# Kernel optimization log

Hardware: AMD Instinct MI355X
Metric: run time of the kernel (lower is better)

The kernel has to match this reference:

```python
import jax, jax.numpy as jnp
import numpy as np

D = 1024      # in_dim
HS = 64       # head_size
H = 16        # num_heads
B, S = 2, 2048


def setup_inputs() -> dict:
    key = jax.random.key(0)
    k1, k2, k3, k4, k5, k6 = jax.random.split(key, 6)
    scale = 1.0 / np.sqrt(D)
    x = jax.random.normal(k1, (B, S, D), dtype=jnp.float32)
    # Stacked per-head projection weights (torch Linear weight is [out,in];
    # random init so layout only needs to be consistent). query weight exists
    # in the torch module but is never used (source bug), so it is omitted.
    Wk = jax.random.normal(k2, (H, D, HS), dtype=jnp.float32) * scale
    Wv = jax.random.normal(k3, (H, D, HS), dtype=jnp.float32) * scale
    Wproj = jax.random.normal(k4, (H * HS, D), dtype=jnp.float32) * (1.0 / np.sqrt(H * HS))
    bproj = jax.random.normal(k5, (D,), dtype=jnp.float32) * 0.01
    return {"x": x, "Wk": Wk, "Wv": Wv, "Wproj": Wproj, "bproj": bproj}


def reference(x, Wk, Wv, Wproj, bproj):
    # Faithful to source: k = key(x); q = value(x); v = value(x)  (q == v, no softmax)
    k = jnp.einsum("bsd,hde->bhse", x, Wk)   # [B,H,S,HS]
    v = jnp.einsum("bsd,hde->bhse", x, Wv)   # [B,H,S,HS]
    q = v
    inv_sqrt = jnp.asarray(HS, x.dtype) ** -0.5
    wei = jnp.einsum("bhse,bhte->bhst", q, k) * inv_sqrt  # [B,H,S,S], unnormalized
    out = jnp.einsum("bhst,bhte->bhse", wei, v)            # [B,H,S,HS]
    # concat heads: [B,S,H*HS]
    out = jnp.transpose(out, (0, 2, 1, 3)).reshape(x.shape[0], x.shape[1], H * HS)
    return out @ Wproj + bproj  # [B,S,D]
```

## Files before the change

### kernel.cpp

```cpp
#include <hip/hip_runtime.h>

#define B_ 2
#define S_ 2048
#define D_ 1024
#define H_ 16
#define HS_ 64
#define HD_ 1024
#define BS_ (B_*S_)
#define KS_ 64
#define TP2_ 264

typedef __attribute__((ext_vector_type(8))) short short8_t;
typedef __attribute__((ext_vector_type(4))) float float4_t;

__device__ inline unsigned short f32_to_bf16(float f) {
  unsigned int u = __float_as_uint(f);
  u += 0x7FFF + ((u >> 16) & 1);
  return (unsigned short)(u >> 16);
}

__device__ inline void async_copy16(const void* g, void* lds) {
  __builtin_amdgcn_global_load_lds(
      (const __attribute__((address_space(1))) void*)g,
      (__attribute__((address_space(3))) void*)lds, 16, 0, 0);
}

#define WAITV6 asm volatile("s_waitcnt vmcnt(6)" ::: "memory")
#define WAITV4 asm volatile("s_waitcnt vmcnt(4)" ::: "memory")
#define WAITV0 asm volatile("s_waitcnt vmcnt(0)" ::: "memory")
#define WAITL0 asm volatile("s_waitcnt lgkmcnt(0)" ::: "memory")
#define BAR    __builtin_amdgcn_s_barrier()
#define SCHEDB __builtin_amdgcn_sched_barrier(0)
#define PRIO1  __builtin_amdgcn_s_setprio(1)
#define PRIO0  __builtin_amdgcn_s_setprio(0)


__global__ __launch_bounds__(256) void prep_kernel(
    const float* __restrict__ x, const float* __restrict__ Wk,
    const float* __restrict__ Wv, unsigned short* __restrict__ xb,
    unsigned short* __restrict__ Wkvt) {
  const int blk = blockIdx.x;
  const int tid = threadIdx.x;
  __shared__ float lds[64][65];
  if (blk < 4096) {
    int idx = blk * 256 + tid;
    float4 v = ((const float4*)x)[idx];
    ushort4 o;
    o.x = f32_to_bf16(v.x); o.y = f32_to_bf16(v.y);
    o.z = f32_to_bf16(v.z); o.w = f32_to_bf16(v.w);
    ((ushort4*)xb)[idx] = o;
    return;
  }
  const int wblk = blk - 4096;
  const int h = wblk >> 4;
  const int d0 = (wblk & 15) * 64;
#pragma unroll
  for (int i = 0; i < 16; ++i) {
    int idx = tid + i * 256; int dd = idx >> 6, e = idx & 63;
    lds[e][dd] = Wk[((size_t)h * D_ + d0 + dd) * HS_ + e];
  }
  __syncthreads();
#pragma unroll
  for (int i = 0; i < 16; ++i) {
    int idx = tid + i * 256; int e = idx >> 6, dd = idx & 63;
    Wkvt[((size_t)h * 128 + e) * D_ + d0 + dd] = f32_to_bf16(lds[e][dd]);
  }
  __syncthreads();
#pragma unroll
  for (int i = 0; i < 16; ++i) {
    int idx = tid + i * 256; int dd = idx >> 6, e = idx & 63;
    lds[e][dd] = Wv[((size_t)h * D_ + d0 + dd) * HS_ + e];
  }
  __syncthreads();
#pragma unroll
  for (int i = 0; i < 16; ++i) {
    int idx = tid + i * 256; int e = idx >> 6, dd = idx & 63;
    Wkvt[((size_t)h * 128 + 64 + e) * D_ + d0 + dd] = f32_to_bf16(lds[e][dd]);
  }
}

__global__ __launch_bounds__(512) void kv_mfma_kernel(
    const unsigned short* __restrict__ xb,
    const unsigned short* __restrict__ Wkvt,
    unsigned short* __restrict__ Vb,
    float* __restrict__ Mpart) {
  const int blk = blockIdx.x;
  const int stile = blk & 15;
  const int h = blk >> 4;
  const int s0 = stile * 256;
  const int tid = threadIdx.x;
  const int lane = tid & 63;
  const int wid = tid >> 6;
  const int wm = wid >> 1, wn = wid & 1;
  const int quad = lane >> 4, l16 = lane & 15;
  const int xa = l16 & 7;

  __shared__ __align__(16) unsigned char smem[147456];
  unsigned short* const Ktl = (unsigned short*)smem;
  unsigned short* const Vtl = (unsigned short*)(smem + 64 * TP2_ * 2);

  float4_t acc[4][4];
  const float4_t fz = {0.f, 0.f, 0.f, 0.f};
#pragma unroll
  for (int i = 0; i < 4; ++i)
#pragma unroll
    for (int j = 0; j < 4; ++j) acc[i][j] = fz;

  unsigned short* pc = (unsigned short*)(smem);
  unsigned short* pn = (unsigned short*)(smem + 49152);
  unsigned short* ps = (unsigned short*)(smem + 98304);

  auto stageu = [&](unsigned short* slot, int kt, int u) {
    const int k0 = kt * KS_;
    if (u < 4) {
      int rb = u * 64 + wid * 8;
      int r = rb + (lane >> 3);
      int ch = ((lane & 7) ^ (r & 7)) * 8;
      async_copy16(xb + (size_t)(s0 + r) * D_ + k0 + ch, slot + rb * KS_);
    } else {
      int rb = (u - 4) * 64 + wid * 8;
      int r = rb + (lane >> 3);
      int ch = ((lane & 7) ^ (r & 7)) * 8;
      async_copy16(Wkvt + ((size_t)h * 128 + r) * D_ + k0 + ch,
                   slot + 16384 + rb * KS_);
    }
  };
  auto rdA = [&](const unsigned short* P, int mi, int ks) {
    return *(const short8_t*)(P + (wm * 64 + mi * 16 + l16) * KS_ +
                              ((ks * 4 + quad) ^ xa) * 8);
  };
  auto rdB = [&](const unsigned short* P, int ni, int ks) {
    return *(const short8_t*)(P + 16384 + (wn * 64 + ni * 16 + l16) * KS_ +
                              ((ks * 4 + quad) ^ xa) * 8);
  };

  short8_t a0[4], a1[4], b0[4], b1[4];

#pragma unroll
  for (int u = 0; u < 6; ++u) stageu(pc, 0, u);
#pragma unroll
  for (int u = 0; u < 6; ++u) stageu(pn, 1, u);
  WAITV6;
  BAR;
#pragma unroll
  for (int mi = 0; mi < 4; ++mi) a0[mi] = rdA(pc, mi, 0);
  b0[0] = rdB(pc, 0, 0); b0[1] = rdB(pc, 1, 0);

  for (int kt = 0; kt < 16; ++kt) {
    const bool st = (kt < 14);
    if (st) { stageu(ps, kt + 2, 0); stageu(ps, kt + 2, 1); }
    BAR; WAITL0; SCHEDB;
    PRIO1;
#pragma unroll
    for (int mi = 0; mi < 4; ++mi) {
      acc[mi][0] = __builtin_amdgcn_mfma_f32_16x16x32_bf16(a0[mi], b0[0], acc[mi][0], 0, 0, 0);
      acc[mi][1] = __builtin_amdgcn_mfma_f32_16x16x32_bf16(a0[mi], b0[1], acc[mi][1], 0, 0, 0);
    }
    PRIO0;
    b0[2] = rdB(pc, 2, 0); b0[3] = rdB(pc, 3, 0);
    if (st) { stageu(ps, kt + 2, 2); stageu(ps, kt + 2, 3); }
    BAR; WAITL0; SCHEDB;
    PRIO1;
#pragma unroll
    for (int mi = 0; mi < 4; ++mi) {
      acc[mi][2] = __builtin_amdgcn_mfma_f32_16x16x32_bf16(a0[mi], b0[2], acc[mi][2], 0, 0, 0);
      acc[mi][3] = __builtin_amdgcn_mfma_f32_16x16x32_bf16(a0[mi], b0[3], acc[mi][3], 0, 0, 0);
    }
    PRIO0;
#pragma unroll
    for (int mi = 0; mi < 4; ++mi) a1[mi] = rdA(pc, mi, 1);
    b1[0] = rdB(pc, 0, 1); b1[1] = rdB(pc, 1, 1);
    if (st) stageu(ps, kt + 2, 4);
    BAR; WAITL0; SCHEDB;
    PRIO1;
#pragma unroll
    for (int mi = 0; mi < 4; ++mi) {
      acc[mi][0] = __builtin_amdgcn_mfma_f32_16x16x32_bf16(a1[mi], b1[0], acc[mi][0], 0, 0, 0);
      acc[mi][1] = __builtin_amdgcn_mfma_f32_16x16x32_bf16(a1[mi], b1[1], acc[mi][1], 0, 0, 0);
    }
    PRIO0;
    b1[2] = rdB(pc, 2, 1); b1[3] = rdB(pc, 3, 1);
    if (st) stageu(ps, kt + 2, 5);
    if (kt < 14) { WAITV6; } else if (kt == 14) { WAITV0; }
    BAR; WAITL0; SCHEDB;
    PRIO1;
#pragma unroll
    for (int mi = 0; mi < 4; ++mi) {
      acc[mi][2] = __builtin_amdgcn_mfma_f32_16x16x32_bf16(a1[mi], b1[2], acc[mi][2], 0, 0, 0);
      acc[mi][3] = __builtin_amdgcn_mfma_f32_16x16x32_bf16(a1[mi], b1[3], acc[mi][3], 0, 0, 0);
    }
    PRIO0;
    if (kt < 15) {
#pragma unroll
      for (int mi = 0; mi < 4; ++mi) a0[mi] = rdA(pn, mi, 0);
      b0[0] = rdB(pn, 0, 0); b0[1] = rdB(pn, 1, 0);
    }
    unsigned short* t = pc; pc = pn; pn = ps; ps = t;
  }
  __syncthreads();

  {
    unsigned short* dstT = (wn == 0) ? Ktl : Vtl;
#pragma unroll
    for (int mi = 0; mi < 4; ++mi)
#pragma unroll
      for (int ni = 0; ni < 4; ++ni) {
        int f = ni * 16 + l16;
        int sm = wm * 64 + mi * 16 + quad * 4;
        ushort4 o;
        o.x = f32_to_bf16(acc[mi][ni][0]);
        o.y = f32_to_bf16(acc[mi][ni][1]);
        o.z = f32_to_bf16(acc[mi][ni][2]);
        o.w = f32_to_bf16(acc[mi][ni][3]);
        *(ushort4*)&dstT[f * TP2_ + sm] = o;
      }
  }
  __syncthreads();

#pragma unroll
  for (int u = 0; u < 4; ++u) {
    int unit = tid + u * 512;
    int s = unit & 255;
    int ec = (unit >> 8) * 8;
    union { unsigned short u16[8]; uint4 v; } tv;
#pragma unroll
    for (int e = 0; e < 8; ++e) tv.u16[e] = Vtl[(ec + e) * TP2_ + s];
    *(uint4*)&Vb[(size_t)(s0 + s) * HD_ + h * 64 + ec] = tv.v;
  }

  {
    const int half = wid >> 2, fq = wid & 3;
    float4_t macc[4];
#pragma unroll
    for (int ni = 0; ni < 4; ++ni) macc[ni] = fz;
#pragma unroll
    for (int ss = 0; ss < 4; ++ss) {
      short8_t ka = *(const short8_t*)&Ktl[(fq * 16 + l16) * TP2_ +
                                           half * 128 + ss * 32 + quad * 8];
#pragma unroll
      for (int ni = 0; ni < 4; ++ni) {
        short8_t vv = *(const short8_t*)&Vtl[(ni * 16 + l16) * TP2_ +
                                             half * 128 + ss * 32 + quad * 8];
        macc[ni] = __builtin_amdgcn_mfma_f32_16x16x32_bf16(ka, vv, macc[ni], 0, 0, 0);
      }
    }
    float* mdst = Mpart + (((size_t)(stile * 2 + half)) * H_ + h) * 4096;
#pragma unroll
    for (int ni = 0; ni < 4; ++ni) {
      int e = ni * 16 + l16;
#pragma unroll
      for (int r = 0; r < 4; ++r) {
        int f = fq * 16 + quad * 4 + r;
        mdst[f * 64 + e] = macc[ni][r];
      }
    }
  }
}

__global__ __launch_bounds__(256) void m_reduce_kernel(
    const float* __restrict__ Mpart, float* __restrict__ M) {
  const int gid = blockIdx.x * 256 + threadIdx.x;
  const int e0 = gid * 4;
  const int bh = e0 >> 12;
  const int idx = e0 & 4095;
  const int b = bh >> 4, h = bh & 15;
  float4 s = {0.f, 0.f, 0.f, 0.f};
#pragma unroll
  for (int p = 0; p < 16; ++p) {
    const float4 v =
        *(const float4*)&Mpart[(((size_t)(b * 16 + p)) * H_ + h) * 4096 + idx];
    s.x += v.x; s.y += v.y; s.z += v.z; s.w += v.w;
  }
  s.x *= 0.125f; s.y *= 0.125f; s.z *= 0.125f; s.w *= 0.125f;
  *(float4*)&M[(size_t)bh * 4096 + idx] = s;
}

__global__ __launch_bounds__(256) void p_kernel(
    const float* __restrict__ M, const float* __restrict__ Wproj,
    unsigned short* __restrict__ Pt) {
  const int blk = blockIdx.x;
  const int dtile = blk & 15;
  const int h = (blk >> 4) & 15;
  const int b = blk >> 8;
  const int d0 = dtile * 64;
  const int tid = threadIdx.x;
  const int tx = tid & 15, ty = tid >> 4;
  __shared__ float Ms[64][68];
  __shared__ float Ws[64][68];
  const size_t mbase = ((size_t)(b * H_ + h)) * HS_ * HS_;
#pragma unroll
  for (int i = 0; i < 16; ++i) {
    int idx = tid + i * 256;
    int f = idx >> 6, e = idx & 63;
    Ms[e][f] = M[mbase + idx];
    Ws[f][e] = Wproj[(size_t)(h * HS_ + f) * D_ + d0 + e];
  }
  __syncthreads();
  float acc[4][4] = {};
#pragma unroll
  for (int kk = 0; kk < 64; ++kk) {
    const float4 a4 = *(const float4*)&Ms[kk][ty * 4];
    const float4 b4 = *(const float4*)&Ws[kk][tx * 4];
    const float a[4] = {a4.x, a4.y, a4.z, a4.w};
    const float bb[4] = {b4.x, b4.y, b4.z, b4.w};
#pragma unroll
    for (int i = 0; i < 4; ++i)
#pragma unroll
      for (int j = 0; j < 4; ++j) acc[i][j] += a[i] * bb[j];
  }
  __syncthreads();
#pragma unroll
  for (int i = 0; i < 4; ++i)
#pragma unroll
    for (int j = 0; j < 4; ++j)
      Ms[tx * 4 + j][ty * 4 + i] = acc[i][j];
  __syncthreads();
  {
    int c = tid >> 2, ch = tid & 3;
    unsigned short* dst = Pt + ((size_t)(b * D_ + d0 + c)) * HD_ + h * 64 + ch * 16;
#pragma unroll
    for (int e = 0; e < 16; ++e) dst[e] = f32_to_bf16(Ms[c][ch * 16 + e]);
  }
}

__global__ __launch_bounds__(512) void out_mfma_kernel(
    const unsigned short* __restrict__ Vb,
    const unsigned short* __restrict__ Pt,
    const float* __restrict__ bproj,
    float* __restrict__ out) {
  const int blk = blockIdx.x;
  const int ntile = blk & 7;
  const int stile = blk >> 3;
  const int s0 = stile * 128;
  const int n0 = ntile * 128;
  const int b = s0 >> 11;
  const int tid = threadIdx.x;
  const int lane = tid & 63;
  const int wid = tid >> 6;
  const int wm = wid & 1, wn = wid >> 1;
  const int quad = lane >> 4, l16 = lane & 15;
  const int xa = l16 & 7;

  __shared__ __align__(16) unsigned char smem[98304];

  float4_t acc[4][2];
  const float4_t fz = {0.f, 0.f, 0.f, 0.f};
#pragma unroll
  for (int i = 0; i < 4; ++i)
#pragma unroll
    for (int j = 0; j < 2; ++j) acc[i][j] = fz;

  const unsigned short* Bpanel = Pt + (size_t)b * D_ * HD_;

  unsigned short* pc = (unsigned short*)(smem);
  unsigned short* pn = (unsigned short*)(smem + 32768);
  unsigned short* ps = (unsigned short*)(smem + 65536);

  auto stageu = [&](unsigned short* slot, int kt, int u) {
    const int k0 = kt * KS_;
    if (u < 2) {
      int rb = u * 64 + wid * 8;
      int r = rb + (lane >> 3);
      int ch = ((lane & 7) ^ (r & 7)) * 8;
      async_copy16(Vb + (size_t)(s0 + r) * HD_ + k0 + ch, slot + rb * KS_);
    } else {
      int rb = (u - 2) * 64 + wid * 8;
      int r = rb + (lane >> 3);
      int ch = ((lane & 7) ^ (r & 7)) * 8;
      async_copy16(Bpanel + (size_t)(n0 + r) * HD_ + k0 + ch,
                   slot + 8192 + rb * KS_);
    }
  };
  auto rdA = [&](const unsigned short* P, int mi, int ks) {
    return *(const short8_t*)(P + (wm * 64 + mi * 16 + l16) * KS_ +
                              ((ks * 4 + quad) ^ xa) * 8);
  };
  auto rdB = [&](const unsigned short* P, int ni, int ks) {
    return *(const short8_t*)(P + 8192 + (wn * 32 + ni * 16 + l16) * KS_ +
                              ((ks * 4 + quad) ^ xa) * 8);
  };

  short8_t a0[4], a1[4], b0[2], b1[2];

#pragma unroll
  for (int u = 0; u < 4; ++u) stageu(pc, 0, u);
#pragma unroll
  for (int u = 0; u < 4; ++u) stageu(pn, 1, u);
  WAITV4;
  BAR;
#pragma unroll
  for (int mi = 0; mi < 4; ++mi) a0[mi] = rdA(pc, mi, 0);
  b0[0] = rdB(pc, 0, 0); b0[1] = rdB(pc, 1, 0);

  for (int kt = 0; kt < 16; ++kt) {
    const bool st = (kt < 14);
    if (st) { stageu(ps, kt + 2, 0); stageu(ps, kt + 2, 1); }
    BAR; WAITL0; SCHEDB;
    PRIO1;
#pragma unroll
    for (int mi = 0; mi < 4; ++mi) {
      acc[mi][0] = __builtin_amdgcn_mfma_f32_16x16x32_bf16(a0[mi], b0[0], acc[mi][0], 0, 0, 0);
      acc[mi][1] = __builtin_amdgcn_mfma_f32_16x16x32_bf16(a0[mi], b0[1], acc[mi][1], 0, 0, 0);
    }
    PRIO0;
#pragma unroll
    for (int mi = 0; mi < 4; ++mi) a1[mi] = rdA(pc, mi, 1);
    b1[0] = rdB(pc, 0, 1); b1[1] = rdB(pc, 1, 1);
    if (st) { stageu(ps, kt + 2, 2); stageu(ps, kt + 2, 3); }
    if (kt < 14) { WAITV4; } else if (kt == 14) { WAITV0; }
    BAR; WAITL0; SCHEDB;
    PRIO1;
#pragma unroll
    for (int mi = 0; mi < 4; ++mi) {
      acc[mi][0] = __builtin_amdgcn_mfma_f32_16x16x32_bf16(a1[mi], b1[0], acc[mi][0], 0, 0, 0);
      acc[mi][1] = __builtin_amdgcn_mfma_f32_16x16x32_bf16(a1[mi], b1[1], acc[mi][1], 0, 0, 0);
    }
    PRIO0;
    if (kt < 15) {
#pragma unroll
      for (int mi = 0; mi < 4; ++mi) a0[mi] = rdA(pn, mi, 0);
      b0[0] = rdB(pn, 0, 0); b0[1] = rdB(pn, 1, 0);
    }
    unsigned short* t = pc; pc = pn; pn = ps; ps = t;
  }

#pragma unroll
  for (int ni = 0; ni < 2; ++ni) {
    int col = n0 + wn * 32 + ni * 16 + l16;
    float bias = bproj[col];
#pragma unroll
    for (int mi = 0; mi < 4; ++mi) {
      int rowb = s0 + wm * 64 + mi * 16 + quad * 4;
#pragma unroll
      for (int r = 0; r < 4; ++r)
        out[(size_t)(rowb + r) * D_ + col] = acc[mi][ni][r] + bias;
    }
  }
}

extern "C" void kernel_launch(void* const* d_in, const int* in_sizes, int n_in,
                              void* d_out, int out_size, void* d_ws, size_t ws_size,
                              hipStream_t stream) {
  const float* x = (const float*)d_in[0];
  const float* Wk = (const float*)d_in[1];
  const float* Wv = (const float*)d_in[2];
  const float* Wproj = (const float*)d_in[3];
  const float* bproj = (const float*)d_in[4];
  float* out = (float*)d_out;

  char* ws = (char*)d_ws;
  unsigned short* xb = (unsigned short*)ws;
  unsigned short* Wkvt = xb + (size_t)BS_ * D_;
  unsigned short* Vb = Wkvt + (size_t)H_ * 128 * D_;
  float* Mpart = (float*)(Vb + (size_t)BS_ * HD_);
  float* M = Mpart + (size_t)32 * H_ * 4096;
  unsigned short* Pt = (unsigned short*)(M + (size_t)B_ * H_ * 4096);

  prep_kernel<<<dim3(4096 + H_ * (D_ / 64)), dim3(256), 0, stream>>>(x, Wk, Wv, xb, Wkvt);
  kv_mfma_kernel<<<dim3(16 * H_), dim3(512), 0, stream>>>(xb, Wkvt, Vb, Mpart);
  m_reduce_kernel<<<dim3(128), dim3(256), 0, stream>>>(Mpart, M);
  p_kernel<<<dim3(B_ * H_ * (D_ / 64)), dim3(256), 0, stream>>>(M, Wproj, Pt);
  out_mfma_kernel<<<dim3(32 * 8), dim3(512), 0, stream>>>(Vb, Pt, bproj, out);
}
```

Baseline: 129.0 us.

## Fuse five kernels into one cooperative persistent kernel with grid syncs

Merges the prep, KV projection, M reduction, P computation and output GEMM kernels into one cooperative launch of 256 blocks of 512 threads, with grid.sync() between stages. Each stage's work is remapped onto the fixed grid, for example the prep stage now loops over 8 chunks per thread and the P stage runs two virtual blocks per workgroup. This removes four kernel launch boundaries and their drain and fill gaps. In exchange it adds grid-wide barrier cost and lower parallelism in the lightweight stages, and it needs all 256 blocks to be co-resident, each holding 147 KB of LDS.

```diff
diff --git a/kernel.cpp b/kernel.cpp
--- a/kernel.cpp
+++ b/kernel.cpp
@@ -1,4 +1,7 @@
 #include <hip/hip_runtime.h>
+#include <hip/hip_cooperative_groups.h>
+
+namespace cg = cooperative_groups;
 
 #define B_ 2
 #define S_ 2048
@@ -35,405 +38,405 @@
 #define PRIO0  __builtin_amdgcn_s_setprio(0)
 
 
-__global__ __launch_bounds__(256) void prep_kernel(
+__global__ __launch_bounds__(512) void fused_kernel(
     const float* __restrict__ x, const float* __restrict__ Wk,
-    const float* __restrict__ Wv, unsigned short* __restrict__ xb,
-    unsigned short* __restrict__ Wkvt) {
+    const float* __restrict__ Wv, const float* __restrict__ Wproj,
+    const float* __restrict__ bproj,
+    unsigned short* __restrict__ xb,
+    unsigned short* __restrict__ Wkvt,
+    unsigned short* __restrict__ Vb,
+    float* __restrict__ Mpart,
+    float* __restrict__ M,
+    unsigned short* __restrict__ Pt,
+    float* __restrict__ out) {
   const int blk = blockIdx.x;
   const int tid = threadIdx.x;
-  __shared__ float lds[64][65];
-  if (blk < 4096) {
-    int idx = blk * 256 + tid;
-    float4 v = ((const float4*)x)[idx];
-    ushort4 o;
-    o.x = f32_to_bf16(v.x); o.y = f32_to_bf16(v.y);
-    o.z = f32_to_bf16(v.z); o.w = f32_to_bf16(v.w);
-    ((ushort4*)xb)[idx] = o;
-    return;
+  __shared__ __align__(16) unsigned char smem[147456];
+  cg::grid_group grid = cg::this_grid();
+
+  {
+#pragma unroll
+    for (int u = 0; u < 8; ++u) {
+      int idx = (blk * 512 + tid) + u * 131072;
+      float4 v = ((const float4*)x)[idx];
+      ushort4 o;
+      o.x = f32_to_bf16(v.x); o.y = f32_to_bf16(v.y);
+      o.z = f32_to_bf16(v.z); o.w = f32_to_bf16(v.w);
+      ((ushort4*)xb)[idx] = o;
+    }
+    float (*lds)[65] = (float(*)[65])smem;
+    const int h = blk >> 4;
+    const int d0 = (blk & 15) * 64;
+#pragma unroll
+    for (int i = 0; i < 8; ++i) {
+      int idx = tid + i * 512; int dd = idx >> 6, e = idx & 63;
+      lds[e][dd] = Wk[((size_t)h * D_ + d0 + dd) * HS_ + e];
+    }
+    __syncthreads();
+#pragma unroll
+    for (int i = 0; i < 8; ++i) {
+      int idx = tid + i * 512; int e = idx >> 6, dd = idx & 63;
+      Wkvt[((size_t)h * 128 + e) * D_ + d0 + dd] = f32_to_bf16(lds[e][dd]);
+    }
+    __syncthreads();
+#pragma unroll
+    for (int i = 0; i < 8; ++i) {
+      int idx = tid + i * 512; int dd = idx >> 6, e = idx & 63;
+      lds[e][dd] = Wv[((size_t)h * D_ + d0 + dd) * HS_ + e];
+    }
+    __syncthreads();
+#pragma unroll
+    for (int i = 0; i < 8; ++i) {
+      int idx = tid + i * 512; int e = idx >> 6, dd = idx & 63;
+      Wkvt[((size_t)h * 128 + 64 + e) * D_ + d0 + dd] = f32_to_bf16(lds[e][dd]);
+    }
   }
-  const int wblk = blk - 4096;
-  const int h = wblk >> 4;
-  const int d0 = (wblk & 15) * 64;
-#pragma unroll
-  for (int i = 0; i < 16; ++i) {
-    int idx = tid + i * 256; int dd = idx >> 6, e = idx & 63;
-    lds[e][dd] = Wk[((size_t)h * D_ + d0 + dd) * HS_ + e];
+  grid.sync();
+
+  {
+    const int stile = blk & 15;
+    const int h = blk >> 4;
+    const int s0 = stile * 256;
+    const int lane = tid & 63;
+    const int wid = tid >> 6;
+    const int wm = wid >> 1, wn = wid & 1;
+    const int quad = lane >> 4, l16 = lane & 15;
+    const int xa = l16 & 7;
+
+    unsigned short* const Ktl = (unsigned short*)smem;
+    unsigned short* const Vtl = (unsigned short*)(smem + 64 * TP2_ * 2);
+
+    float4_t acc[4][4];
+    const float4_t fz = {0.f, 0.f, 0.f, 0.f};
+#pragma unroll
+    for (int i = 0; i < 4; ++i)
+#pragma unroll
+      for (int j = 0; j < 4; ++j) acc[i][j] = fz;
+
+    unsigned short* pc = (unsigned short*)(smem);
+    unsigned short* pn = (unsigned short*)(smem + 49152);
+    unsigned short* ps = (unsigned short*)(smem + 98304);
+
+    auto stageu = [&](unsigned short* slot, int kt, int u) {
+      const int k0 = kt * KS_;
+      if (u < 4) {
+        int rb = u * 64 + wid * 8;
+        int r = rb + (lane >> 3);
+        int ch = ((lane & 7) ^ (r & 7)) * 8;
+        async_copy16(xb + (size_t)(s0 + r) * D_ + k0 + ch, slot + rb * KS_);
+      } else {
+        int rb = (u - 4) * 64 + wid * 8;
+        int r = rb + (lane >> 3);
+        int ch = ((lane & 7) ^ (r & 7)) * 8;
+        async_copy16(Wkvt + ((size_t)h * 128 + r) * D_ + k0 + ch,
+                     slot + 16384 + rb * KS_);
+      }
+    };
+    auto rdA = [&](const unsigned short* P, int mi, int ks) {
+      return *(const short8_t*)(P + (wm * 64 + mi * 16 + l16) * KS_ +
+                                ((ks * 4 + quad) ^ xa) * 8);
+    };
+    auto rdB = [&](const unsigned short* P, int ni, int ks) {
+      return *(const short8_t*)(P + 16384 + (wn * 64 + ni * 16 + l16) * KS_ +
+                                ((ks * 4 + quad) ^ xa) * 8);
+    };
+
+    short8_t a0[4], a1[4], b0[4], b1[4];
+
+#pragma unroll
+    for (int u = 0; u < 6; ++u) stageu(pc, 0, u);
+#pragma unroll
+    for (int u = 0; u < 6; ++u) stageu(pn, 1, u);
+    WAITV6;
+    BAR;
+#pragma unroll
+    for (int mi = 0; mi < 4; ++mi) a0[mi] = rdA(pc, mi, 0);
+    b0[0] = rdB(pc, 0, 0); b0[1] = rdB(pc, 1, 0);
+
+    for (int kt = 0; kt < 16; ++kt) {
+      const bool st = (kt < 14);
+      if (st) { stageu(ps, kt + 2, 0); stageu(ps, kt + 2, 1); }
+      BAR; WAITL0; SCHEDB;
+      PRIO1;
+#pragma unroll
+      for (int mi = 0; mi < 4; ++mi) {
+        acc[mi][0] = __builtin_amdgcn_mfma_f32_16x16x32_bf16(a0[mi], b0[0], acc[mi][0], 0, 0, 0);
+        acc[mi][1] = __builtin_amdgcn_mfma_f32_16x16x32_bf16(a0[mi], b0[1], acc[mi][1], 0, 0, 0);
+      }
+      PRIO0;
+      b0[2] = rdB(pc, 2, 0); b0[3] = rdB(pc, 3, 0);
+      if (st) { stageu(ps, kt + 2, 2); stageu(ps, kt + 2, 3); }
+      BAR; WAITL0; SCHEDB;
+      PRIO1;
+#pragma unroll
+      for (int mi = 0; mi < 4; ++mi) {
+        acc[mi][2] = __builtin_amdgcn_mfma_f32_16x16x32_bf16(a0[mi], b0[2], acc[mi][2], 0, 0, 0);
+        acc[mi][3] = __builtin_amdgcn_mfma_f32_16x16x32_bf16(a0[mi], b0[3], acc[mi][3], 0, 0, 0);
+      }
+      PRIO0;
+#pragma unroll
+      for (int mi = 0; mi < 4; ++mi) a1[mi] = rdA(pc, mi, 1);
+      b1[0] = rdB(pc, 0, 1); b1[1] = rdB(pc, 1, 1);
+      if (st) stageu(ps, kt + 2, 4);
+      BAR; WAITL0; SCHEDB;
+      PRIO1;
+#pragma unroll
+      for (int mi = 0; mi < 4; ++mi) {
+        acc[mi][0] = __builtin_amdgcn_mfma_f32_16x16x32_bf16(a1[mi], b1[0], acc[mi][0], 0, 0, 0);
+        acc[mi][1] = __builtin_amdgcn_mfma_f32_16x16x32_bf16(a1[mi], b1[1], acc[mi][1], 0, 0, 0);
+      }
+      PRIO0;
+      b1[2] = rdB(pc, 2, 1); b1[3] = rdB(pc, 3, 1);
+      if (st) stageu(ps, kt + 2, 5);
+      if (kt < 14) { WAITV6; } else if (kt == 14) { WAITV0; }
+      BAR; WAITL0; SCHEDB;
+      PRIO1;
+#pragma unroll
+      for (int mi = 0; mi < 4; ++mi) {
+        acc[mi][2] = __builtin_amdgcn_mfma_f32_16x16x32_bf16(a1[mi], b1[2], acc[mi][2], 0, 0, 0);
+        acc[mi][3] = __builtin_amdgcn_mfma_f32_16x16x32_bf16(a1[mi], b1[3], acc[mi][3], 0, 0, 0);
+      }
+      PRIO0;
+      if (kt < 15) {
+#pragma unroll
+        for (int mi = 0; mi < 4; ++mi) a0[mi] = rdA(pn, mi, 0);
+        b0[0] = rdB(pn, 0, 0); b0[1] = rdB(pn, 1, 0);
+      }
+      unsigned short* t = pc; pc = pn; pn = ps; ps = t;
+    }
+    __syncthreads();
+
+    {
+      unsigned short* dstT = (wn == 0) ? Ktl : Vtl;
+#pragma unroll
+      for (int mi = 0; mi < 4; ++mi)
+#pragma unroll
+        for (int ni = 0; ni < 4; ++ni) {
+          int f = ni * 16 + l16;
+          int sm = wm * 64 + mi * 16 + quad * 4;
+          ushort4 o;
+          o.x = f32_to_bf16(acc[mi][ni][0]);
+          o.y = f32_to_bf16(acc[mi][ni][1]);
+          o.z = f32_to_bf16(acc[mi][ni][2]);
+          o.w = f32_to_bf16(acc[mi][ni][3]);
+          *(ushort4*)&dstT[f * TP2_ + sm] = o;
+        }
+    }
+    __syncthreads();
+
+#pragma unroll
+    for (int u = 0; u < 4; ++u) {
+      int unit = tid + u * 512;
+      int s = unit & 255;
+      int ec = (unit >> 8) * 8;
+      union { unsigned short u16[8]; uint4 v; } tv;
+#pragma unroll
+      for (int e = 0; e < 8; ++e) tv.u16[e] = Vtl[(ec + e) * TP2_ + s];
+      *(uint4*)&Vb[(size_t)(s0 + s) * HD_ + h * 64 + ec] = tv.v;
+    }
+
+    {
+      const int half = wid >> 2, fq = wid & 3;
+      float4_t macc[4];
+#pragma unroll
+      for (int ni = 0; ni < 4; ++ni) macc[ni] = fz;
+#pragma unroll
+      for (int ss = 0; ss < 4; ++ss) {
+        short8_t ka = *(const short8_t*)&Ktl[(fq * 16 + l16) * TP2_ +
+                                             half * 128 + ss * 32 + quad * 8];
+#pragma unroll
+        for (int ni = 0; ni < 4; ++ni) {
+          short8_t vv = *(const short8_t*)&Vtl[(ni * 16 + l16) * TP2_ +
+                                               half * 128 + ss * 32 + quad * 8];
+          macc[ni] = __builtin_amdgcn_mfma_f32_16x16x32_bf16(ka, vv, macc[ni], 0, 0, 0);
+        }
+      }
+      float* mdst = Mpart + (((size_t)(stile * 2 + half)) * H_ + h) * 4096;
+#pragma unroll
+      for (int ni = 0; ni < 4; ++ni) {
+        int e = ni * 16 + l16;
+#pragma unroll
+        for (int r = 0; r < 4; ++r) {
+          int f = fq * 16 + quad * 4 + r;
+          mdst[f * 64 + e] = macc[ni][r];
+        }
+      }
+    }
   }
-  __syncthreads();
-#pragma unroll
-  for (int i = 0; i < 16; ++i) {
-    int idx = tid + i * 256; int e = idx >> 6, dd = idx & 63;
-    Wkvt[((size_t)h * 128 + e) * D_ + d0 + dd] = f32_to_bf16(lds[e][dd]);
+  grid.sync();
+
+  {
+    int gid = blk * 512 + tid;
+    if (gid < 32768) {
+      const int e0 = gid * 4;
+      const int bh = e0 >> 12;
+      const int idx = e0 & 4095;
+      const int b = bh >> 4, h = bh & 15;
+      float4 s = {0.f, 0.f, 0.f, 0.f};
+#pragma unroll
+      for (int p = 0; p < 16; ++p) {
+        const float4 v =
+            *(const float4*)&Mpart[(((size_t)(b * 16 + p)) * H_ + h) * 4096 + idx];
+        s.x += v.x; s.y += v.y; s.z += v.z; s.w += v.w;
+      }
+      s.x *= 0.125f; s.y *= 0.125f; s.z *= 0.125f; s.w *= 0.125f;
+      *(float4*)&M[(size_t)bh * 4096 + idx] = s;
+    }
   }
-  __syncthreads();
-#pragma unroll
-  for (int i = 0; i < 16; ++i) {
-    int idx = tid + i * 256; int dd = idx >> 6, e = idx & 63;
-    lds[e][dd] = Wv[((size_t)h * D_ + d0 + dd) * HS_ + e];
+  grid.sync();
+
+  {
+    const int sel = tid >> 8;
+    const int tid2 = tid & 255;
+    const int vb = blk * 2 + sel;
+    const int dtile = vb & 15;
+    const int h = (vb >> 4) & 15;
+    const int b = vb >> 8;
+    const int d0 = dtile * 64;
+    const int tx = tid2 & 15, ty = tid2 >> 4;
+    float (*Ms)[68] = (float(*)[68])(smem + (size_t)sel * 34816);
+    float (*Ws)[68] = (float(*)[68])(smem + (size_t)sel * 34816 + 17408);
+    const size_t mbase = ((size_t)(b * H_ + h)) * HS_ * HS_;
+#pragma unroll
+    for (int i = 0; i < 16; ++i) {
+      int idx = tid2 + i * 256;
+      int f = idx >> 6, e = idx & 63;
+      Ms[e][f] = M[mbase + idx];
+      Ws[f][e] = Wproj[(size_t)(h * HS_ + f) * D_ + d0 + e];
+    }
+    __syncthreads();
+    float acc[4][4] = {};
+#pragma unroll
+    for (int kk = 0; kk < 64; ++kk) {
+      const float4 a4 = *(const float4*)&Ms[kk][ty * 4];
+      const float4 b4 = *(const float4*)&Ws[kk][tx * 4];
+      const float a[4] = {a4.x, a4.y, a4.z, a4.w};
+      const float bb[4] = {b4.x, b4.y, b4.z, b4.w};
+#pragma unroll
+      for (int i = 0; i < 4; ++i)
+#pragma unroll
+        for (int j = 0; j < 4; ++j) acc[i][j] += a[i] * bb[j];
+    }
+    __syncthreads();
+#pragma unroll
+    for (int i = 0; i < 4; ++i)
+#pragma unroll
+      for (int j = 0; j < 4; ++j)
+        Ms[tx * 4 + j][ty * 4 + i] = acc[i][j];
+    __syncthreads();
+    {
+      int c = tid2 >> 2, ch = tid2 & 3;
+      unsigned short* dst = Pt + ((size_t)(b * D_ + d0 + c)) * HD_ + h * 64 + ch * 16;
+#pragma unroll
+      for (int e = 0; e < 16; ++e) dst[e] = f32_to_bf16(Ms[c][ch * 16 + e]);
+    }
   }
-  __syncthreads();
-#pragma unroll
-  for (int i = 0; i < 16; ++i) {
-    int idx = tid + i * 256; int e = idx >> 6, dd = idx & 63;
-    Wkvt[((size_t)h * 128 + 64 + e) * D_ + d0 + dd] = f32_to_bf16(lds[e][dd]);
-  }
-}
-
-__global__ __launch_bounds__(512) void kv_mfma_kernel(
-    const unsigned short* __restrict__ xb,
-    const unsigned short* __restrict__ Wkvt,
-    unsigned short* __restrict__ Vb,
-    float* __restrict__ Mpart) {
-  const int blk = blockIdx.x;
-  const int stile = blk & 15;
-  const int h = blk >> 4;
-  const int s0 = stile * 256;
-  const int tid = threadIdx.x;
-  const int lane = tid & 63;
-  const int wid = tid >> 6;
-  const int wm = wid >> 1, wn = wid & 1;
-  const int quad = lane >> 4, l16 = lane & 15;
-  const int xa = l16 & 7;
-
-  __shared__ __align__(16) unsigned char smem[147456];
-  unsigned short* const Ktl = (unsigned short*)smem;
-  unsigned short* const Vtl = (unsigned short*)(smem + 64 * TP2_ * 2);
-
-  float4_t acc[4][4];
-  const float4_t fz = {0.f, 0.f, 0.f, 0.f};
-#pragma unroll
-  for (int i = 0; i < 4; ++i)
-#pragma unroll
-    for (int j = 0; j < 4; ++j) acc[i][j] = fz;
-
-  unsigned short* pc = (unsigned short*)(smem);
-  unsigned short* pn = (unsigned short*)(smem + 49152);
-  unsigned short* ps = (unsigned short*)(smem + 98304);
-
-  auto stageu = [&](unsigned short* slot, int kt, int u) {
-    const int k0 = kt * KS_;
-    if (u < 4) {
-      int rb = u * 64 + wid * 8;
-      int r = rb + (lane >> 3);
-      int ch = ((lane & 7) ^ (r & 7)) * 8;
-      async_copy16(xb + (size_t)(s0 + r) * D_ + k0 + ch, slot + rb * KS_);
-    } else {
-      int rb = (u - 4) * 64 + wid * 8;
-      int r = rb + (lane >> 3);
-      int ch = ((lane & 7) ^ (r & 7)) * 8;
-      async_copy16(Wkvt + ((size_t)h * 128 + r) * D_ + k0 + ch,
-                   slot + 16384 + rb * KS_);
-    }
-  };
-  auto rdA = [&](const unsigned short* P, int mi, int ks) {
-    return *(const short8_t*)(P + (wm * 64 + mi * 16 + l16) * KS_ +
-                              ((ks * 4 + quad) ^ xa) * 8);
-  };
-  auto rdB = [&](const unsigned short* P, int ni, int ks) {
-    return *(const short8_t*)(P + 16384 + (wn * 64 + ni * 16 + l16) * KS_ +
-                              ((ks * 4 + quad) ^ xa) * 8);
-  };
-
-  short8_t a0[4], a1[4], b0[4], b1[4];
-
-#pragma unroll
-  for (int u = 0; u < 6; ++u) stageu(pc, 0, u);
-#pragma unroll
-  for (int u = 0; u < 6; ++u) stageu(pn, 1, u);
-  WAITV6;
-  BAR;
-#pragma unroll
-  for (int mi = 0; mi < 4; ++mi) a0[mi] = rdA(pc, mi, 0);
-  b0[0] = rdB(pc, 0, 0); b0[1] = rdB(pc, 1, 0);
-
-  for (int kt = 0; kt < 16; ++kt) {
-    const bool st = (kt < 14);
-    if (st) { stageu(ps, kt + 2, 0); stageu(ps, kt + 2, 1); }
-    BAR; WAITL0; SCHEDB;
-    PRIO1;
-#pragma unroll
-    for (int mi = 0; mi < 4; ++mi) {
-      acc[mi][0] = __builtin_amdgcn_mfma_f32_16x16x32_bf16(a0[mi], b0[0], acc[mi][0], 0, 0, 0);
-      acc[mi][1] = __builtin_amdgcn_mfma_f32_16x16x32_bf16(a0[mi], b0[1], acc[mi][1], 0, 0, 0);
-    }
-    PRIO0;
-    b0[2] = rdB(pc, 2, 0); b0[3] = rdB(pc, 3, 0);
-    if (st) { stageu(ps, kt + 2, 2); stageu(ps, kt + 2, 3); }
-    BAR; WAITL0; SCHEDB;
-    PRIO1;
-#pragma unroll
-    for (int mi = 0; mi < 4; ++mi) {
-      acc[mi][2] = __builtin_amdgcn_mfma_f32_16x16x32_bf16(a0[mi], b0[2], acc[mi][2], 0, 0, 0);
-      acc[mi][3] = __builtin_amdgcn_mfma_f32_16x16x32_bf16(a0[mi], b0[3], acc[mi][3], 0, 0, 0);
-    }
-    PRIO0;
-#pragma unroll
-    for (int mi = 0; mi < 4; ++mi) a1[mi] = rdA(pc, mi, 1);
-    b1[0] = rdB(pc, 0, 1); b1[1] = rdB(pc, 1, 1);
-    if (st) stageu(ps, kt + 2, 4);
-    BAR; WAITL0; SCHEDB;
-    PRIO1;
-#pragma unroll
-    for (int mi = 0; mi < 4; ++mi) {
-      acc[mi][0] = __builtin_amdgcn_mfma_f32_16x16x32_bf16(a1[mi], b1[0], acc[mi][0], 0, 0, 0);
-      acc[mi][1] = __builtin_amdgcn_mfma_f32_16x16x32_bf16(a1[mi], b1[1], acc[mi][1], 0, 0, 0);
-    }
-    PRIO0;
-    b1[2] = rdB(pc, 2, 1); b1[3] = rdB(pc, 3, 1);
-    if (st) stageu(ps, kt + 2, 5);
-    if (kt < 14) { WAITV6; } else if (kt == 14) { WAITV0; }
-    BAR; WAITL0; SCHEDB;
-    PRIO1;
-#pragma unroll
-    for (int mi = 0; mi < 4; ++mi) {
-      acc[mi][2] = __builtin_amdgcn_mfma_f32_16x16x32_bf16(a1[mi], b1[2], acc[mi][2], 0, 0, 0);
-      acc[mi][3] = __builtin_amdgcn_mfma_f32_16x16x32_bf16(a1[mi], b1[3], acc[mi][3], 0, 0, 0);
-    }
-    PRIO0;
-    if (kt < 15) {
-#pragma unroll
-      for (int mi = 0; mi < 4; ++mi) a0[mi] = rdA(pn, mi, 0);
-      b0[0] = rdB(pn, 0, 0); b0[1] = rdB(pn, 1, 0);
-    }
-    unsigned short* t = pc; pc = pn; pn = ps; ps = t;
-  }
-  __syncthreads();
+  grid.sync();
 
   {
-    unsigned short* dstT = (wn == 0) ? Ktl : Vtl;
-#pragma unroll
-    for (int mi = 0; mi < 4; ++mi)
-#pragma unroll
-      for (int ni = 0; ni < 4; ++ni) {
-        int f = ni * 16 + l16;
-        int sm = wm * 64 + mi * 16 + quad * 4;
-        ushort4 o;
-        o.x = f32_to_bf16(acc[mi][ni][0]);
-        o.y = f32_to_bf16(acc[mi][ni][1]);
-        o.z = f32_to_bf16(acc[mi][ni][2]);
-        o.w = f32_to_bf16(acc[mi][ni][3]);
-        *(ushort4*)&dstT[f * TP2_ + sm] = o;
-      }
-  }
-  __syncthreads();
-
-#pragma unroll
-  for (int u = 0; u < 4; ++u) {
-    int unit = tid + u * 512;
-    int s = unit & 255;
-    int ec = (unit >> 8) * 8;
-    union { unsigned short u16[8]; uint4 v; } tv;
-#pragma unroll
-    for (int e = 0; e < 8; ++e) tv.u16[e] = Vtl[(ec + e) * TP2_ + s];
-    *(uint4*)&Vb[(size_t)(s0 + s) * HD_ + h * 64 + ec] = tv.v;
-  }
-
-  {
-    const int half = wid >> 2, fq = wid & 3;
-    float4_t macc[4];
-#pragma unroll
-    for (int ni = 0; ni < 4; ++ni) macc[ni] = fz;
-#pragma unroll
-    for (int ss = 0; ss < 4; ++ss) {
-      short8_t ka = *(const short8_t*)&Ktl[(fq * 16 + l16) * TP2_ +
-                                           half * 128 + ss * 32 + quad * 8];
-#pragma unroll
-      for (int ni = 0; ni < 4; ++ni) {
-        short8_t vv = *(const short8_t*)&Vtl[(ni * 16 + l16) * TP2_ +
-                                             half * 128 + ss * 32 + quad * 8];
-        macc[ni] = __builtin_amdgcn_mfma_f32_16x16x32_bf16(ka, vv, macc[ni], 0, 0, 0);
-      }
-    }
-    float* mdst = Mpart + (((size_t)(stile * 2 + half)) * H_ + h) * 4096;
-#pragma unroll
-    for (int ni = 0; ni < 4; ++ni) {
-      int e = ni * 16 + l16;
-#pragma unroll
-      for (int r = 0; r < 4; ++r) {
-        int f = fq * 16 + quad * 4 + r;
-        mdst[f * 64 + e] = macc[ni][r];
-      }
-    }
-  }
-}
-
-__global__ __launch_bounds__(256) void m_reduce_kernel(
-    const float* __restrict__ Mpart, float* __restrict__ M) {
-  const int gid = blockIdx.x * 256 + threadIdx.x;
-  const int e0 = gid * 4;
-  const int bh = e0 >> 12;
-  const int idx = e0 & 4095;
-  const int b = bh >> 4, h = bh & 15;
-  float4 s = {0.f, 0.f, 0.f, 0.f};
-#pragma unroll
-  for (int p = 0; p < 16; ++p) {
-    const float4 v =
-        *(const float4*)&Mpart[(((size_t)(b * 16 + p)) * H_ + h) * 4096 + idx];
-    s.x += v.x; s.y += v.y; s.z += v.z; s.w += v.w;
-  }
-  s.x *= 0.125f; s.y *= 0.125f; s.z *= 0.125f; s.w *= 0.125f;
-  *(float4*)&M[(size_t)bh * 4096 + idx] = s;
-}
-
-__global__ __launch_bounds__(256) void p_kernel(
-    const float* __restrict__ M, const float* __restrict__ Wproj,
-    unsigned short* __restrict__ Pt) {
-  const int blk = blockIdx.x;
-  const int dtile = blk & 15;
-  const int h = (blk >> 4) & 15;
-  const int b = blk >> 8;
-  const int d0 = dtile * 64;
-  const int tid = threadIdx.x;
-  const int tx = tid & 15, ty = tid >> 4;
-  __shared__ float Ms[64][68];
-  __shared__ float Ws[64][68];
-  const size_t mbase = ((size_t)(b * H_ + h)) * HS_ * HS_;
-#pragma unroll
-  for (int i = 0; i < 16; ++i) {
-    int idx = tid + i * 256;
-    int f = idx >> 6, e = idx & 63;
-    Ms[e][f] = M[mbase + idx];
-    Ws[f][e] = Wproj[(size_t)(h * HS_ + f) * D_ + d0 + e];
-  }
-  __syncthreads();
-  float acc[4][4] = {};
-#pragma unroll
-  for (int kk = 0; kk < 64; ++kk) {
-    const float4 a4 = *(const float4*)&Ms[kk][ty * 4];
-    const float4 b4 = *(const float4*)&Ws[kk][tx * 4];
-    const float a[4] = {a4.x, a4.y, a4.z, a4.w};
-    const float bb[4] = {b4.x, b4.y, b4.z, b4.w};
+    const int ntile = blk & 7;
+    const int stile = blk >> 3;
+    const int s0 = stile * 128;
+    const int n0 = ntile * 128;
+    const int b = s0 >> 11;
+    const int lane = tid & 63;
+    const int wid = tid >> 6;
+    const int wm = wid & 1, wn = wid >> 1;
+    const int quad = lane >> 4, l16 = lane & 15;
+    const int xa = l16 & 7;
+
+    float4_t acc[4][2];
+    const float4_t fz = {0.f, 0.f, 0.f, 0.f};
 #pragma unroll
     for (int i = 0; i < 4; ++i)
 #pragma unroll
-      for (int j = 0; j < 4; ++j) acc[i][j] += a[i] * bb[j];
-  }
-  __syncthreads();
-#pragma unroll
-  for (int i = 0; i < 4; ++i)
-#pragma unroll
-    for (int j = 0; j < 4; ++j)
-      Ms[tx * 4 + j][ty * 4 + i] = acc[i][j];
-  __syncthreads();
-  {
-    int c = tid >> 2, ch = tid & 3;
-    unsigned short* dst = Pt + ((size_t)(b * D_ + d0 + c)) * HD_ + h * 64 + ch * 16;
-#pragma unroll
-    for (int e = 0; e < 16; ++e) dst[e] = f32_to_bf16(Ms[c][ch * 16 + e]);
-  }
-}
-
-__global__ __launch_bounds__(512) void out_mfma_kernel(
-    const unsigned short* __restrict__ Vb,
-    const unsigned short* __restrict__ Pt,
-    const float* __restrict__ bproj,
-    float* __restrict__ out) {
-  const int blk = blockIdx.x;
-  const int ntile = blk & 7;
-  const int stile = blk >> 3;
-  const int s0 = stile * 128;
-  const int n0 = ntile * 128;
-  const int b = s0 >> 11;
-  const int tid = threadIdx.x;
-  const int lane = tid & 63;
-  const int wid = tid >> 6;
-  const int wm = wid & 1, wn = wid >> 1;
-  const int quad = lane >> 4, l16 = lane & 15;
-  const int xa = l16 & 7;
-
-  __shared__ __align__(16) unsigned char smem[98304];
-
-  float4_t acc[4][2];
-  const float4_t fz = {0.f, 0.f, 0.f, 0.f};
-#pragma unroll
-  for (int i = 0; i < 4; ++i)
-#pragma unroll
-    for (int j = 0; j < 2; ++j) acc[i][j] = fz;
-
-  const unsigned short* Bpanel = Pt + (size_t)b * D_ * HD_;
-
-  unsigned short* pc = (unsigned short*)(smem);
-  unsigned short* pn = (unsigned short*)(smem + 32768);
-  unsigned short* ps = (unsigned short*)(smem + 65536);
-
-  auto stageu = [&](unsigned short* slot, int kt, int u) {
-    const int k0 = kt * KS_;
-    if (u < 2) {
-      int rb = u * 64 + wid * 8;
-      int r = rb + (lane >> 3);
-      int ch = ((lane & 7) ^ (r & 7)) * 8;
-      async_copy16(Vb + (size_t)(s0 + r) * HD_ + k0 + ch, slot + rb * KS_);
-    } else {
-      int rb = (u - 2) * 64 + wid * 8;
-      int r = rb + (lane >> 3);
-      int ch = ((lane & 7) ^ (r & 7)) * 8;
-      async_copy16(Bpanel + (size_t)(n0 + r) * HD_ + k0 + ch,
-                   slot + 8192 + rb * KS_);
-    }
-  };
-  auto rdA = [&](const unsigned short* P, int mi, int ks) {
-    return *(const short8_t*)(P + (wm * 64 + mi * 16 + l16) * KS_ +
-                              ((ks * 4 + quad) ^ xa) * 8);
-  };
-  auto rdB = [&](const unsigned short* P, int ni, int ks) {
-    return *(const short8_t*)(P + 8192 + (wn * 32 + ni * 16 + l16) * KS_ +
-                              ((ks * 4 + quad) ^ xa) * 8);
-  };
-
-  short8_t a0[4], a1[4], b0[2], b1[2];
-
-#pragma unroll
-  for (int u = 0; u < 4; ++u) stageu(pc, 0, u);
-#pragma unroll
-  for (int u = 0; u < 4; ++u) stageu(pn, 1, u);
-  WAITV4;
-  BAR;
-#pragma unroll
-  for (int mi = 0; mi < 4; ++mi) a0[mi] = rdA(pc, mi, 0);
-  b0[0] = rdB(pc, 0, 0); b0[1] = rdB(pc, 1, 0);
-
-  for (int kt = 0; kt < 16; ++kt) {
-    const bool st = (kt < 14);
-    if (st) { stageu(ps, kt + 2, 0); stageu(ps, kt + 2, 1); }
-    BAR; WAITL0; SCHEDB;
-    PRIO1;
-#pragma unroll
-    for (int mi = 0; mi < 4; ++mi) {
-      acc[mi][0] = __builtin_amdgcn_mfma_f32_16x16x32_bf16(a0[mi], b0[0], acc[mi][0], 0, 0, 0);
-      acc[mi][1] = __builtin_amdgcn_mfma_f32_16x16x32_bf16(a0[mi], b0[1], acc[mi][1], 0, 0, 0);
-    }
-    PRIO0;
-#pragma unroll
-    for (int mi = 0; mi < 4; ++mi) a1[mi] = rdA(pc, mi, 1);
-    b1[0] = rdB(pc, 0, 1); b1[1] = rdB(pc, 1, 1);
-    if (st) { stageu(ps, kt + 2, 2); stageu(ps, kt + 2, 3); }
-    if (kt < 14) { WAITV4; } else if (kt == 14) { WAITV0; }
-    BAR; WAITL0; SCHEDB;
-    PRIO1;
-#pragma unroll
-    for (int mi = 0; mi < 4; ++mi) {
-      acc[mi][0] = __builtin_amdgcn_mfma_f32_16x16x32_bf16(a1[mi], b1[0], acc[mi][0], 0, 0, 0);
-      acc[mi][1] = __builtin_amdgcn_mfma_f32_16x16x32_bf16(a1[mi], b1[1], acc[mi][1], 0, 0, 0);
-    }
-    PRIO0;
-    if (kt < 15) {
-#pragma unroll
-      for (int mi = 0; mi < 4; ++mi) a0[mi] = rdA(pn, mi, 0);
-      b0[0] = rdB(pn, 0, 0); b0[1] = rdB(pn, 1, 0);
-    }
-    unsigned short* t = pc; pc = pn; pn = ps; ps = t;
-  }
-
-#pragma unroll
-  for (int ni = 0; ni < 2; ++ni) {
-    int col = n0 + wn * 32 + ni * 16 + l16;
-    float bias = bproj[col];
-#pragma unroll
-    for (int mi = 0; mi < 4; ++mi) {
-      int rowb = s0 + wm * 64 + mi * 16 + quad * 4;
-#pragma unroll
-      for (int r = 0; r < 4; ++r)
-        out[(size_t)(rowb + r) * D_ + col] = acc[mi][ni][r] + bias;
+      for (int j = 0; j < 2; ++j) acc[i][j] = fz;
+
+    const unsigned short* Bpanel = Pt + (size_t)b * D_ * HD_;
+
+    unsigned short* pc = (unsigned short*)(smem);
+    unsigned short* pn = (unsigned short*)(smem + 32768);
+    unsigned short* ps = (unsigned short*)(smem + 65536);
+
+    auto stageu = [&](unsigned short* slot, int kt, int u) {
+      const int k0 = kt * KS_;
+      if (u < 2) {
+        int rb = u * 64 + wid * 8;
+        int r = rb + (lane >> 3);
+        int ch = ((lane & 7) ^ (r & 7)) * 8;
+        async_copy16(Vb + (size_t)(s0 + r) * HD_ + k0 + ch, slot + rb * KS_);
+      } else {
+        int rb = (u - 2) * 64 + wid * 8;
+        int r = rb + (lane >> 3);
+        int ch = ((lane & 7) ^ (r & 7)) * 8;
+        async_copy16(Bpanel + (size_t)(n0 + r) * HD_ + k0 + ch,
+                     slot + 8192 + rb * KS_);
+      }
+    };
+    auto rdA = [&](const unsigned short* P, int mi, int ks) {
+      return *(const short8_t*)(P + (wm * 64 + mi * 16 + l16) * KS_ +
+                                ((ks * 4 + quad) ^ xa) * 8);
+    };
+    auto rdB = [&](const unsigned short* P, int ni, int ks) {
+      return *(const short8_t*)(P + 8192 + (wn * 32 + ni * 16 + l16) * KS_ +
+                                ((ks * 4 + quad) ^ xa) * 8);
+    };
+
+    short8_t a0[4], a1[4], b0[2], b1[2];
+
+#pragma unroll
+    for (int u = 0; u < 4; ++u) stageu(pc, 0, u);
+#pragma unroll
+    for (int u = 0; u < 4; ++u) stageu(pn, 1, u);
+    WAITV4;
+    BAR;
+#pragma unroll
+    for (int mi = 0; mi < 4; ++mi) a0[mi] = rdA(pc, mi, 0);
+    b0[0] = rdB(pc, 0, 0); b0[1] = rdB(pc, 1, 0);
+
+    for (int kt = 0; kt < 16; ++kt) {
+      const bool st = (kt < 14);
+      if (st) { stageu(ps, kt + 2, 0); stageu(ps, kt + 2, 1); }
+      BAR; WAITL0; SCHEDB;
+      PRIO1;
+#pragma unroll
+      for (int mi = 0; mi < 4; ++mi) {
+        acc[mi][0] = __builtin_amdgcn_mfma_f32_16x16x32_bf16(a0[mi], b0[0], acc[mi][0], 0, 0, 0);
+        acc[mi][1] = __builtin_amdgcn_mfma_f32_16x16x32_bf16(a0[mi], b0[1], acc[mi][1], 0, 0, 0);
+      }
+      PRIO0;
+#pragma unroll
+      for (int mi = 0; mi < 4; ++mi) a1[mi] = rdA(pc, mi, 1);
+      b1[0] = rdB(pc, 0, 1); b1[1] = rdB(pc, 1, 1);
+      if (st) { stageu(ps, kt + 2, 2); stageu(ps, kt + 2, 3); }
+      if (kt < 14) { WAITV4; } else if (kt == 14) { WAITV0; }
+      BAR; WAITL0; SCHEDB;
+      PRIO1;
+#pragma unroll
+      for (int mi = 0; mi < 4; ++mi) {
+        acc[mi][0] = __builtin_amdgcn_mfma_f32_16x16x32_bf16(a1[mi], b1[0], acc[mi][0], 0, 0, 0);
+        acc[mi][1] = __builtin_amdgcn_mfma_f32_16x16x32_bf16(a1[mi], b1[1], acc[mi][1], 0, 0, 0);
+      }
+      PRIO0;
+      if (kt < 15) {
+#pragma unroll
+        for (int mi = 0; mi < 4; ++mi) a0[mi] = rdA(pn, mi, 0);
+        b0[0] = rdB(pn, 0, 0); b0[1] = rdB(pn, 1, 0);
+      }
+      unsigned short* t = pc; pc = pn; pn = ps; ps = t;
+    }
+
+#pragma unroll
+    for (int ni = 0; ni < 2; ++ni) {
+      int col = n0 + wn * 32 + ni * 16 + l16;
+      float bias = bproj[col];
+#pragma unroll
+      for (int mi = 0; mi < 4; ++mi) {
+        int rowb = s0 + wm * 64 + mi * 16 + quad * 4;
+#pragma unroll
+        for (int r = 0; r < 4; ++r)
+          out[(size_t)(rowb + r) * D_ + col] = acc[mi][ni][r] + bias;
+      }
     }
   }
 }
@@ -456,9 +459,9 @@
   float* M = Mpart + (size_t)32 * H_ * 4096;
   unsigned short* Pt = (unsigned short*)(M + (size_t)B_ * H_ * 4096);
 
-  prep_kernel<<<dim3(4096 + H_ * (D_ / 64)), dim3(256), 0, stream>>>(x, Wk, Wv, xb, Wkvt);
-  kv_mfma_kernel<<<dim3(16 * H_), dim3(512), 0, stream>>>(xb, Wkvt, Vb, Mpart);
-  m_reduce_kernel<<<dim3(128), dim3(256), 0, stream>>>(Mpart, M);
-  p_kernel<<<dim3(B_ * H_ * (D_ / 64)), dim3(256), 0, stream>>>(M, Wproj, Pt);
-  out_mfma_kernel<<<dim3(32 * 8), dim3(512), 0, stream>>>(Vb, Pt, bproj, out);
+  void* args[] = {(void*)&x,    (void*)&Wk, (void*)&Wv, (void*)&Wproj,
+                  (void*)&bproj, (void*)&xb, (void*)&Wkvt, (void*)&Vb,
+                  (void*)&Mpart, (void*)&M,  (void*)&Pt,   (void*)&out};
+  hipLaunchCooperativeKernel((const void*)fused_kernel, dim3(256), dim3(512),
+                             args, 0, stream);
 }
```

Result: slower. 257.0 us (+99.3%).

## Replace M partial-sum reduction kernel with atomics and remap blocks per XCD

Applied to the files above, without the earlier changes.

Drops the separate m_reduce kernel and the Mpart buffer. kv_mfma_kernel now atomically adds its scaled partial K^T V products straight into M, and prep_kernel zeroes M first. Both MFMA kernels also remap block indices so that s-tiles sharing data land on the same XCD, for better L2 locality. This saves one launch and a round trip through global memory, but adds float atomic contention, 16 adds per element, and nondeterministic summation order.

```diff
diff --git a/kernel.cpp b/kernel.cpp
--- a/kernel.cpp
+++ b/kernel.cpp
@@ -10,6 +10,7 @@
 #define KS_ 64
 #define TP2_ 264
 
+
 typedef __attribute__((ext_vector_type(8))) short short8_t;
 typedef __attribute__((ext_vector_type(4))) float float4_t;
 
@@ -38,7 +39,7 @@
 __global__ __launch_bounds__(256) void prep_kernel(
     const float* __restrict__ x, const float* __restrict__ Wk,
     const float* __restrict__ Wv, unsigned short* __restrict__ xb,
-    unsigned short* __restrict__ Wkvt) {
+    unsigned short* __restrict__ Wkvt, float* __restrict__ M) {
   const int blk = blockIdx.x;
   const int tid = threadIdx.x;
   __shared__ float lds[64][65];
@@ -51,6 +52,12 @@
     ((ushort4*)xb)[idx] = o;
     return;
   }
+  if (blk >= 4352) {
+    int idx = (blk - 4352) * 256 + tid;
+    float4 z = {0.f, 0.f, 0.f, 0.f};
+    ((float4*)M)[idx] = z;
+    return;
+  }
   const int wblk = blk - 4096;
   const int h = wblk >> 4;
   const int d0 = (wblk & 15) * 64;
@@ -83,10 +90,11 @@
     const unsigned short* __restrict__ xb,
     const unsigned short* __restrict__ Wkvt,
     unsigned short* __restrict__ Vb,
-    float* __restrict__ Mpart) {
+    float* __restrict__ M) {
   const int blk = blockIdx.x;
-  const int stile = blk & 15;
-  const int h = blk >> 4;
+  const int xcd = blk & 7, o = blk >> 3;
+  const int stile = xcd * 2 + (o & 1);
+  const int h = o >> 1;
   const int s0 = stile * 256;
   const int tid = threadIdx.x;
   const int lane = tid & 63;
@@ -207,12 +215,12 @@
       for (int ni = 0; ni < 4; ++ni) {
         int f = ni * 16 + l16;
         int sm = wm * 64 + mi * 16 + quad * 4;
-        ushort4 o;
-        o.x = f32_to_bf16(acc[mi][ni][0]);
-        o.y = f32_to_bf16(acc[mi][ni][1]);
-        o.z = f32_to_bf16(acc[mi][ni][2]);
-        o.w = f32_to_bf16(acc[mi][ni][3]);
-        *(ushort4*)&dstT[f * TP2_ + sm] = o;
+        ushort4 o4;
+        o4.x = f32_to_bf16(acc[mi][ni][0]);
+        o4.y = f32_to_bf16(acc[mi][ni][1]);
+        o4.z = f32_to_bf16(acc[mi][ni][2]);
+        o4.w = f32_to_bf16(acc[mi][ni][3]);
+        *(ushort4*)&dstT[f * TP2_ + sm] = o4;
       }
   }
   __syncthreads();
@@ -244,35 +252,18 @@
         macc[ni] = __builtin_amdgcn_mfma_f32_16x16x32_bf16(ka, vv, macc[ni], 0, 0, 0);
       }
     }
-    float* mdst = Mpart + (((size_t)(stile * 2 + half)) * H_ + h) * 4096;
+    const int slot = stile * 2 + half;
+    float* mdst = M + (((size_t)((slot >> 4) * H_ + h)) * 4096);
 #pragma unroll
     for (int ni = 0; ni < 4; ++ni) {
       int e = ni * 16 + l16;
 #pragma unroll
       for (int r = 0; r < 4; ++r) {
         int f = fq * 16 + quad * 4 + r;
-        mdst[f * 64 + e] = macc[ni][r];
+        unsafeAtomicAdd(&mdst[f * 64 + e], 0.125f * macc[ni][r]);
       }
     }
   }
-}
-
-__global__ __launch_bounds__(256) void m_reduce_kernel(
-    const float* __restrict__ Mpart, float* __restrict__ M) {
-  const int gid = blockIdx.x * 256 + threadIdx.x;
-  const int e0 = gid * 4;
-  const int bh = e0 >> 12;
-  const int idx = e0 & 4095;
-  const int b = bh >> 4, h = bh & 15;
-  float4 s = {0.f, 0.f, 0.f, 0.f};
-#pragma unroll
-  for (int p = 0; p < 16; ++p) {
-    const float4 v =
-        *(const float4*)&Mpart[(((size_t)(b * 16 + p)) * H_ + h) * 4096 + idx];
-    s.x += v.x; s.y += v.y; s.z += v.z; s.w += v.w;
-  }
-  s.x *= 0.125f; s.y *= 0.125f; s.z *= 0.125f; s.w *= 0.125f;
-  *(float4*)&M[(size_t)bh * 4096 + idx] = s;
 }
 
 __global__ __launch_bounds__(256) void p_kernel(
@@ -329,8 +320,9 @@
     const float* __restrict__ bproj,
     float* __restrict__ out) {
   const int blk = blockIdx.x;
-  const int ntile = blk & 7;
-  const int stile = blk >> 3;
+  const int xcd = blk & 7, o = blk >> 3;
+  const int stile = xcd * 4 + (o & 3);
+  const int ntile = o >> 2;
   const int s0 = stile * 128;
   const int n0 = ntile * 128;
   const int b = s0 >> 11;
@@ -452,13 +444,12 @@
   unsigned short* xb = (unsigned short*)ws;
   unsigned short* Wkvt = xb + (size_t)BS_ * D_;
   unsigned short* Vb = Wkvt + (size_t)H_ * 128 * D_;
-  float* Mpart = (float*)(Vb + (size_t)BS_ * HD_);
-  float* M = Mpart + (size_t)32 * H_ * 4096;
+  float* M = (float*)(Vb + (size_t)BS_ * HD_);
   unsigned short* Pt = (unsigned short*)(M + (size_t)B_ * H_ * 4096);
 
-  prep_kernel<<<dim3(4096 + H_ * (D_ / 64)), dim3(256), 0, stream>>>(x, Wk, Wv, xb, Wkvt);
-  kv_mfma_kernel<<<dim3(16 * H_), dim3(512), 0, stream>>>(xb, Wkvt, Vb, Mpart);
-  m_reduce_kernel<<<dim3(128), dim3(256), 0, stream>>>(Mpart, M);
+  prep_kernel<<<dim3(4096 + H_ * (D_ / 64) + 128), dim3(256), 0, stream>>>(
+      x, Wk, Wv, xb, Wkvt, M);
+  kv_mfma_kernel<<<dim3(256), dim3(512), 0, stream>>>(xb, Wkvt, Vb, M);
   p_kernel<<<dim3(B_ * H_ * (D_ / 64)), dim3(256), 0, stream>>>(M, Wproj, Pt);
-  out_mfma_kernel<<<dim3(32 * 8), dim3(512), 0, stream>>>(Vb, Pt, bproj, out);
-}
+  out_mfma_kernel<<<dim3(256), dim3(512), 0, stream>>>(Vb, Pt, bproj, out);
+}
```

New measurement: 128.0 us. No clear change (-0.7%).
